# Kernel tuning notes

Hardware: AMD Instinct MI355X
Metric: run time of the kernel (lower is better)

## Reference

```python
import jax, jax.numpy as jnp
import numpy as np
import math

B, S, D, H = 2, 2048, 768, 12
HD = D // H


def setup_inputs() -> dict:
    key = jax.random.key(0)
    ks = jax.random.split(key, 9)
    scale = 1.0 / math.sqrt(D)
    x = jax.random.normal(ks[0], (B, S, D), dtype=jnp.float32)
    # causal mask: True where attention is allowed (query i attends to key j<=i)
    mask = jnp.tril(jnp.ones((S, S), dtype=bool))[None, None]  # [1,1,S,S]
    wq = jax.random.normal(ks[1], (D, D), dtype=jnp.float32) * scale
    bq = jnp.zeros((D,), dtype=jnp.float32)
    wk = jax.random.normal(ks[2], (D, D), dtype=jnp.float32) * scale
    bk = jnp.zeros((D,), dtype=jnp.float32)
    wv = jax.random.normal(ks[3], (D, D), dtype=jnp.float32) * scale
    bv = jnp.zeros((D,), dtype=jnp.float32)
    wo = jax.random.normal(ks[4], (D, D), dtype=jnp.float32) * scale
    bo = jnp.zeros((D,), dtype=jnp.float32)
    return {"x": x, "mask": mask, "wq": wq, "bq": bq, "wk": wk, "bk": bk,
            "wv": wv, "bv": bv, "wo": wo, "bo": bo}


def reference(x, mask, wq, bq, wk, bk, wv, bv, wo, bo):
    b, s, d = x.shape
    # projections (flax Linear: y = x @ kernel + bias)
    q = (x @ wq + bq).reshape(b, s, H, HD).transpose(0, 2, 1, 3)  # [b,h,s,hd]
    k = (x @ wk + bk).reshape(b, s, H, HD).transpose(0, 2, 1, 3)
    v = (x @ wv + bv).reshape(b, s, H, HD).transpose(0, 2, 1, 3)
    scores = jnp.einsum('bhqd,bhkd->bhqk', q, k) / math.sqrt(HD)  # [b,h,s,s]
    scores = jnp.where(mask, scores, -jnp.inf)
    attn = jax.nn.softmax(scores, axis=-1)
    out = jnp.einsum('bhqk,bhkd->bhqd', attn, v)  # [b,h,s,hd]
    out = out.transpose(0, 2, 1, 3).reshape(b, s, d)
    return out @ wo + bo
```

## Files before the change

### kernel.cpp

```cpp
#include <hip/hip_runtime.h>
#include <math.h>

#define BATCH 2
#define SEQ   2048
#define DMODEL 768
#define NHEAD 12
#define HDIM  64

typedef unsigned short u16;
typedef __attribute__((ext_vector_type(8))) short bf16x8;
typedef __attribute__((ext_vector_type(4))) float f32x4;
typedef __attribute__((ext_vector_type(8))) unsigned short us8;
typedef __attribute__((ext_vector_type(4))) unsigned short us4;

__device__ __forceinline__ u16 f2bf(float f) {
    union { float f; unsigned u; } v; v.f = f;
    unsigned u = v.u;
    u += 0x7fff + ((u >> 16) & 1);
    return (u16)(u >> 16);
}

__device__ __forceinline__ void g2l16(const void* g, void* l) {
    __builtin_amdgcn_global_load_lds(
        (const __attribute__((address_space(1))) unsigned int*)g,
        (__attribute__((address_space(3))) unsigned int*)(unsigned int)(unsigned long long)(uintptr_t)l,
        16, 0, 0);
}

__global__ __launch_bounds__(256) void prep(const float* __restrict__ x,
                                            const float* __restrict__ w0,
                                            const float* __restrict__ w1,
                                            const float* __restrict__ w2,
                                            const float* __restrict__ w3,
                                            u16* __restrict__ xb,
                                            u16* __restrict__ Wt_all) {
    __shared__ float t[32][33];
    const int bid = blockIdx.x;
    if (bid < 3072) {
        int i = bid * 256 + threadIdx.x;
        float4 v = ((const float4*)x)[i];
        us4 o;
        o.x = f2bf(v.x); o.y = f2bf(v.y); o.z = f2bf(v.z); o.w = f2bf(v.w);
        *(us4*)&xb[(size_t)i * 4] = o;
    } else {
        const int wid = bid - 3072;
        const int z  = wid / 576;
        const int rr = wid % 576;
        const int by = rr / 24, bx = rr % 24;
        const float* W = z == 0 ? w0 : z == 1 ? w1 : z == 2 ? w2 : w3;
        u16* Wt = Wt_all + (size_t)z * DMODEL * DMODEL;

        int tx = threadIdx.x & 31, ty = threadIdx.x >> 5;
        int xg = bx * 32 + tx;
        #pragma unroll
        for (int j = 0; j < 32; j += 8)
            t[ty + j][tx] = W[(size_t)(by * 32 + ty + j) * DMODEL + xg];
        __syncthreads();
        int x2 = by * 32 + tx;
        #pragma unroll
        for (int j = 0; j < 32; j += 8)
            Wt[(size_t)(bx * 32 + ty + j) * DMODEL + x2] = f2bf(t[tx][ty + j]);
    }
}

__device__ __forceinline__ void mfma_loop(const u16* __restrict__ Ag,
                                          const u16* __restrict__ Bt,
                                          int m0, int n0, int tid,
                                          u16* As, u16* Bs,
                                          f32x4 acc[4][4]) {
    const int lane = tid & 63;
    const int quad = lane >> 4, l16 = lane & 15;
    const int w    = tid >> 6;
    const int wm   = w >> 1, wn = w & 1;
    const int rowA = tid >> 2;
    const int kch  = (tid & 3) * 8;

    for (int k0 = 0; k0 < DMODEL; k0 += 32) {
        const u16* Agk = Ag + (size_t)m0 * DMODEL + k0;
        const u16* Btk = Bt + (size_t)n0 * DMODEL + k0;
        g2l16(Agk + (size_t)rowA * DMODEL + kch,        As + tid * 8);
        g2l16(Agk + (size_t)(rowA + 64) * DMODEL + kch, As + 2048 + tid * 8);
        g2l16(Btk + (size_t)rowA * DMODEL + kch,        Bs + tid * 8);
        g2l16(Btk + (size_t)(rowA + 64) * DMODEL + kch, Bs + 2048 + tid * 8);
        __syncthreads();

        bf16x8 af[4], bfr[4];
        #pragma unroll
        for (int i = 0; i < 4; ++i)
            af[i] = *(const bf16x8*)&As[(wm * 64 + i * 16 + l16) * 32 + quad * 8];
        #pragma unroll
        for (int j = 0; j < 4; ++j)
            bfr[j] = *(const bf16x8*)&Bs[(wn * 64 + j * 16 + l16) * 32 + quad * 8];
        #pragma unroll
        for (int i = 0; i < 4; ++i)
            #pragma unroll
            for (int j = 0; j < 4; ++j)
                acc[i][j] = __builtin_amdgcn_mfma_f32_16x16x32_bf16(af[i], bfr[j], acc[i][j], 0, 0, 0);
        __syncthreads();
    }
}

__global__ __launch_bounds__(256) void gemm_qkv(
    const u16* __restrict__ xb, const u16* __restrict__ WtQK,
    const u16* __restrict__ WtV,
    const float* __restrict__ bq, const float* __restrict__ bk,
    const float* __restrict__ bv,
    u16* __restrict__ QK, u16* __restrict__ Vt) {

    __shared__ __align__(16) u16 As[128 * 32];
    __shared__ __align__(16) u16 Bs[128 * 32];

    const int tid  = threadIdx.x;
    const int lane = tid & 63;
    const int w    = tid >> 6;
    const int quad = lane >> 4, l16 = lane & 15;
    const int wm   = w >> 1, wn = w & 1;
    const int bid  = blockIdx.x;

    f32x4 acc[4][4] = {};

    if (bid < 384) {
        const int m0 = (bid & 31) * 128, n0 = (bid >> 5) * 128;
        mfma_loop(xb, WtQK, m0, n0, tid, As, Bs, acc);

        const size_t n_elem = (size_t)BATCH * SEQ * DMODEL;
        #pragma unroll
        for (int j = 0; j < 4; ++j) {
            const int n     = n0 + wn * 64 + j * 16 + l16;
            const int which = n / 768;
            const int nn    = n - which * 768;
            const float bias  = (which == 0 ? bq : bk)[nn];
            const float scale = (which == 0) ? 0.125f : 1.0f;
            const int h = nn >> 6, hd = nn & 63;
            u16* outw = QK + (size_t)which * n_elem;
            #pragma unroll
            for (int i = 0; i < 4; ++i) {
                const int mbase = m0 + wm * 64 + i * 16 + quad * 4;
                #pragma unroll
                for (int r = 0; r < 4; ++r) {
                    const int m  = mbase + r;
                    const int b_ = m >> 11, s_ = m & 2047;
                    outw[(size_t)((b_ * NHEAD + h) * SEQ + s_) * HDIM + hd] =
                        f2bf((acc[i][j][r] + bias) * scale);
                }
            }
        }
    } else {
        const int vid = bid - 384;
        const int m0 = (vid % 6) * 128, n0 = (vid / 6) * 128;
        mfma_loop(WtV, xb, m0, n0, tid, As, Bs, acc);

        #pragma unroll
        for (int i = 0; i < 4; ++i) {
            const int rbase = m0 + wm * 64 + i * 16 + quad * 4;
            #pragma unroll
            for (int r = 0; r < 4; ++r) {
                const int row_g = rbase + r;
                const float bias = bv[row_g];
                const int h = row_g >> 6, hd = row_g & 63;
                #pragma unroll
                for (int j = 0; j < 4; ++j) {
                    const int col_g = n0 + wn * 64 + j * 16 + l16;
                    const int b_ = col_g >> 11, s_ = col_g & 2047;
                    Vt[(size_t)((b_ * NHEAD + h) * HDIM + hd) * SEQ + s_] =
                        f2bf(acc[i][j][r] + bias);
                }
            }
        }
    }
}

__global__ __launch_bounds__(256) void gemm_out(
    const u16* __restrict__ Ag, const u16* __restrict__ Bt,
    const float* __restrict__ bo, float* __restrict__ out) {

    __shared__ __align__(16) u16 As[128 * 32];
    __shared__ __align__(16) u16 Bs[128 * 32];

    const int tid  = threadIdx.x;
    const int lane = tid & 63;
    const int w    = tid >> 6;
    const int quad = lane >> 4, l16 = lane & 15;
    const int wm   = w >> 1, wn = w & 1;
    const int m0 = blockIdx.x * 128, n0 = blockIdx.y * 128;

    f32x4 acc[4][4] = {};
    mfma_loop(Ag, Bt, m0, n0, tid, As, Bs, acc);

    #pragma unroll
    for (int i = 0; i < 4; ++i) {
        const int mbase = m0 + wm * 64 + i * 16 + quad * 4;
        #pragma unroll
        for (int r = 0; r < 4; ++r) {
            const int m = mbase + r;
            #pragma unroll
            for (int j = 0; j < 4; ++j) {
                const int n = n0 + wn * 64 + j * 16 + l16;
                out[(size_t)m * DMODEL + n] = acc[i][j][r] + bo[n];
            }
        }
    }
}

__global__ __launch_bounds__(256) void flash_attn_mfma(
    const u16* __restrict__ Q, const u16* __restrict__ K,
    const u16* __restrict__ Vt, u16* __restrict__ A) {

    __shared__ __align__(16) u16 Kl[64 * 72];
    __shared__ __align__(16) u16 Vl[64 * 72];
    __shared__ __align__(16) u16 Pl[4][16 * 72];

    const int tid  = threadIdx.x;
    const int lane = tid & 63;
    const int w    = tid >> 6;
    const int quad = lane >> 4;
    const int l16  = lane & 15;

    const int p  = blockIdx.x;
    const int bh = blockIdx.y;
    const int uq = (w < 2) ? p : 63 - p;
    const int wrow0 = uq * 32 + (w & 1) * 16;
    const int wlast = wrow0 + 15;

    const size_t base = (size_t)bh * SEQ * HDIM;
    const u16* Qg = Q + base;
    const u16* Kg = K + base;
    const u16* Vg = Vt + base;

    bf16x8 qf0 = *(const bf16x8*)&Qg[(size_t)(wrow0 + l16) * 64 + quad * 8];
    bf16x8 qf1 = *(const bf16x8*)&Qg[(size_t)(wrow0 + l16) * 64 + quad * 8 + 32];

    f32x4 o[4] = {};
    float l_acc[4] = {0.f, 0.f, 0.f, 0.f};

    const int qrow = wrow0 + quad * 4;
    const int uB = 63 - p;
    const int tcount = (32 * uB + 31) / 64 + 1;

    for (int t2 = 0; t2 < tcount; ++t2) {
        const int j0 = t2 * 64;
        __syncthreads();

        #pragma unroll
        for (int r = 0; r < 2; ++r) {
            int e = tid + r * 256;
            int row = e >> 3, col = (e & 7) * 8;
            *(us8*)&Kl[row * 72 + col] = *(const us8*)&Kg[(size_t)(j0 + row) * 64 + col];
        }
        #pragma unroll
        for (int r = 0; r < 2; ++r) {
            int e = tid + r * 256;
            int d = e >> 3, kc = (e & 7) * 8;
            *(us8*)&Vl[d * 72 + kc] = *(const us8*)&Vg[(size_t)d * SEQ + j0 + kc];
        }
        __syncthreads();

        if (j0 > wlast) continue;

        f32x4 s[4];
        #pragma unroll
        for (int c = 0; c < 4; ++c) {
            bf16x8 kf0 = *(const bf16x8*)&Kl[(c * 16 + l16) * 72 + quad * 8];
            bf16x8 kf1 = *(const bf16x8*)&Kl[(c * 16 + l16) * 72 + quad * 8 + 32];
            f32x4 a2 = {};
            a2 = __builtin_amdgcn_mfma_f32_16x16x32_bf16(qf0, kf0, a2, 0, 0, 0);
            a2 = __builtin_amdgcn_mfma_f32_16x16x32_bf16(qf1, kf1, a2, 0, 0, 0);
            s[c] = a2;
        }

        if (j0 + 63 > wrow0) {
            #pragma unroll
            for (int c = 0; c < 4; ++c) {
                int jg = j0 + c * 16 + l16;
                #pragma unroll
                for (int r = 0; r < 4; ++r)
                    if (jg > qrow + r) s[c][r] = -INFINITY;
            }
        }

        #pragma unroll
        for (int c = 0; c < 4; ++c)
            #pragma unroll
            for (int r = 0; r < 4; ++r)
                s[c][r] = __expf(s[c][r]);
        #pragma unroll
        for (int r = 0; r < 4; ++r)
            l_acc[r] += (s[0][r] + s[1][r]) + (s[2][r] + s[3][r]);

        u16* Pw = Pl[w];
        #pragma unroll
        for (int c = 0; c < 4; ++c)
            #pragma unroll
            for (int r = 0; r < 4; ++r)
                Pw[(quad * 4 + r) * 72 + c * 16 + l16] = f2bf(s[c][r]);
        bf16x8 pf0 = *(const bf16x8*)&Pw[l16 * 72 + quad * 8];
        bf16x8 pf1 = *(const bf16x8*)&Pw[l16 * 72 + quad * 8 + 32];

        #pragma unroll
        for (int c2 = 0; c2 < 4; ++c2) {
            bf16x8 vf0 = *(const bf16x8*)&Vl[(c2 * 16 + l16) * 72 + quad * 8];
            bf16x8 vf1 = *(const bf16x8*)&Vl[(c2 * 16 + l16) * 72 + quad * 8 + 32];
            o[c2] = __builtin_amdgcn_mfma_f32_16x16x32_bf16(pf0, vf0, o[c2], 0, 0, 0);
            o[c2] = __builtin_amdgcn_mfma_f32_16x16x32_bf16(pf1, vf1, o[c2], 0, 0, 0);
        }
    }

    #pragma unroll
    for (int off = 1; off < 16; off <<= 1)
        #pragma unroll
        for (int r = 0; r < 4; ++r)
            l_acc[r] += __shfl_xor(l_acc[r], off);

    const int b = bh / NHEAD, h = bh % NHEAD;
    #pragma unroll
    for (int r = 0; r < 4; ++r) {
        float inv = 1.0f / l_acc[r];
        int sg = qrow + r;
        u16* dst = A + ((size_t)(b * SEQ + sg)) * DMODEL + h * HDIM;
        #pragma unroll
        for (int c2 = 0; c2 < 4; ++c2)
            dst[c2 * 16 + l16] = f2bf(o[c2][r] * inv);
    }
}

extern "C" void kernel_launch(void* const* d_in, const int* in_sizes, int n_in,
                              void* d_out, int out_size, void* d_ws, size_t ws_size,
                              hipStream_t stream) {
    const float* x  = (const float*)d_in[0];
    const float* wq = (const float*)d_in[2];
    const float* bq = (const float*)d_in[3];
    const float* wk = (const float*)d_in[4];
    const float* bk = (const float*)d_in[5];
    const float* wv = (const float*)d_in[6];
    const float* bv = (const float*)d_in[7];
    const float* wo = (const float*)d_in[8];
    const float* bo = (const float*)d_in[9];
    float* out = (float*)d_out;

    const size_t n_elem = (size_t)BATCH * SEQ * DMODEL;
    const size_t w_elem = (size_t)DMODEL * DMODEL;

    u16* xb     = (u16*)d_ws;
    u16* Wt_all = xb + n_elem;
    u16* Qw     = Wt_all + 4 * w_elem;
    u16* Kw     = Qw + n_elem;
    u16* Vtw    = Kw + n_elem;
    u16* Aw     = Vtw + n_elem;

    dim3 blk(256);

    prep<<<dim3(3072 + 2304), blk, 0, stream>>>(x, wq, wk, wv, wo, xb, Wt_all);

    gemm_qkv<<<dim3(384 + 192), blk, 0, stream>>>(xb, Wt_all,
                                                  Wt_all + 2 * w_elem,
                                                  bq, bk, bv, Qw, Vtw);

    flash_attn_mfma<<<dim3(32, 24), blk, 0, stream>>>(Qw, Kw, Vtw, Aw);

    gemm_out<<<dim3(32, 6), blk, 0, stream>>>(Aw, Wt_all + 3 * w_elem, bo, out);
}
```

Before: 193.2 us.

## Restructure flash attention into single-wave blocks and shrink output GEMM tiles

New measurement: 213.6 us. +10.6%, slower.

```diff
diff --git a/kernel.cpp b/kernel.cpp
--- a/kernel.cpp
+++ b/kernel.cpp
@@ -174,152 +174,222 @@
     const u16* __restrict__ Ag, const u16* __restrict__ Bt,
     const float* __restrict__ bo, float* __restrict__ out) {
 
-    __shared__ __align__(16) u16 As[128 * 32];
-    __shared__ __align__(16) u16 Bs[128 * 32];
+    __shared__ __align__(16) u16 As[64 * 32];
+    __shared__ __align__(16) u16 Bs[64 * 32];
 
     const int tid  = threadIdx.x;
     const int lane = tid & 63;
     const int w    = tid >> 6;
     const int quad = lane >> 4, l16 = lane & 15;
     const int wm   = w >> 1, wn = w & 1;
-    const int m0 = blockIdx.x * 128, n0 = blockIdx.y * 128;
-
-    f32x4 acc[4][4] = {};
-    mfma_loop(Ag, Bt, m0, n0, tid, As, Bs, acc);
+    const int m0 = blockIdx.x * 64, n0 = blockIdx.y * 64;
+
+    const int rowA = tid >> 2;
+    const int kch  = (tid & 3) * 8;
+
+    f32x4 acc[2][2] = {};
+
+    for (int k0 = 0; k0 < DMODEL; k0 += 32) {
+        g2l16(Ag + (size_t)(m0 + rowA) * DMODEL + k0 + kch, As + tid * 8);
+        g2l16(Bt + (size_t)(n0 + rowA) * DMODEL + k0 + kch, Bs + tid * 8);
+        __syncthreads();
+
+        bf16x8 af[2], bfr[2];
+        #pragma unroll
+        for (int i = 0; i < 2; ++i)
+            af[i] = *(const bf16x8*)&As[(wm * 32 + i * 16 + l16) * 32 + quad * 8];
+        #pragma unroll
+        for (int j = 0; j < 2; ++j)
+            bfr[j] = *(const bf16x8*)&Bs[(wn * 32 + j * 16 + l16) * 32 + quad * 8];
+        #pragma unroll
+        for (int i = 0; i < 2; ++i)
+            #pragma unroll
+            for (int j = 0; j < 2; ++j)
+                acc[i][j] = __builtin_amdgcn_mfma_f32_16x16x32_bf16(af[i], bfr[j], acc[i][j], 0, 0, 0);
+        __syncthreads();
+    }
 
     #pragma unroll
-    for (int i = 0; i < 4; ++i) {
-        const int mbase = m0 + wm * 64 + i * 16 + quad * 4;
+    for (int i = 0; i < 2; ++i) {
+        const int mbase = m0 + wm * 32 + i * 16 + quad * 4;
         #pragma unroll
         for (int r = 0; r < 4; ++r) {
             const int m = mbase + r;
             #pragma unroll
-            for (int j = 0; j < 4; ++j) {
-                const int n = n0 + wn * 64 + j * 16 + l16;
+            for (int j = 0; j < 2; ++j) {
+                const int n = n0 + wn * 32 + j * 16 + l16;
                 out[(size_t)m * DMODEL + n] = acc[i][j][r] + bo[n];
             }
         }
     }
 }
 
-__global__ __launch_bounds__(256) void flash_attn_mfma(
+__global__ __launch_bounds__(64) void flash_attn_mfma(
     const u16* __restrict__ Q, const u16* __restrict__ K,
     const u16* __restrict__ Vt, u16* __restrict__ A) {
 
-    __shared__ __align__(16) u16 Kl[64 * 72];
-    __shared__ __align__(16) u16 Vl[64 * 72];
-    __shared__ __align__(16) u16 Pl[4][16 * 72];
-
-    const int tid  = threadIdx.x;
-    const int lane = tid & 63;
-    const int w    = tid >> 6;
+    __shared__ __align__(16) u16 Pl[16 * 72];
+
+    const int lane = threadIdx.x;
     const int quad = lane >> 4;
     const int l16  = lane & 15;
 
-    const int p  = blockIdx.x;
-    const int bh = blockIdx.y;
-    const int uq = (w < 2) ? p : 63 - p;
-    const int wrow0 = uq * 32 + (w & 1) * 16;
-    const int wlast = wrow0 + 15;
+    const int bid = blockIdx.x;
+    const int j   = bid >> 8;
+    const int c   = bid & 255;
+    const int v   = c & 63;
+    const int g   = c >> 6;
+    const int bh  = j * 4 + g;
+    const int rot = (j >> 1) * 21;
+    const int vr  = (v + rot) & 63;
+    const int u   = (j & 1) ? (63 - vr) : vr;
+
+    const int rs = u * 16;
+    const int rb = 2032 - rs;
+    const int slast = rs + 15;
 
     const size_t base = (size_t)bh * SEQ * HDIM;
     const u16* Qg = Q + base;
     const u16* Kg = K + base;
     const u16* Vg = Vt + base;
 
-    bf16x8 qf0 = *(const bf16x8*)&Qg[(size_t)(wrow0 + l16) * 64 + quad * 8];
-    bf16x8 qf1 = *(const bf16x8*)&Qg[(size_t)(wrow0 + l16) * 64 + quad * 8 + 32];
-
-    f32x4 o[4] = {};
-    float l_acc[4] = {0.f, 0.f, 0.f, 0.f};
-
-    const int qrow = wrow0 + quad * 4;
-    const int uB = 63 - p;
-    const int tcount = (32 * uB + 31) / 64 + 1;
-
-    for (int t2 = 0; t2 < tcount; ++t2) {
+    bf16x8 qs0 = *(const bf16x8*)&Qg[(size_t)(rs + l16) * 64 + quad * 8];
+    bf16x8 qs1 = *(const bf16x8*)&Qg[(size_t)(rs + l16) * 64 + quad * 8 + 32];
+    bf16x8 qb0 = *(const bf16x8*)&Qg[(size_t)(rb + l16) * 64 + quad * 8];
+    bf16x8 qb1 = *(const bf16x8*)&Qg[(size_t)(rb + l16) * 64 + quad * 8 + 32];
+
+    f32x4 ob[4] = {}, os[4] = {};
+    float lb[4] = {0.f, 0.f, 0.f, 0.f};
+    float ls[4] = {0.f, 0.f, 0.f, 0.f};
+
+    const int tc = ((rb + 15) >> 6) + 1;
+
+    for (int t2 = 0; t2 < tc; ++t2) {
         const int j0 = t2 * 64;
-        __syncthreads();
-
-        #pragma unroll
-        for (int r = 0; r < 2; ++r) {
-            int e = tid + r * 256;
-            int row = e >> 3, col = (e & 7) * 8;
-            *(us8*)&Kl[row * 72 + col] = *(const us8*)&Kg[(size_t)(j0 + row) * 64 + col];
-        }
-        #pragma unroll
-        for (int r = 0; r < 2; ++r) {
-            int e = tid + r * 256;
-            int d = e >> 3, kc = (e & 7) * 8;
-            *(us8*)&Vl[d * 72 + kc] = *(const us8*)&Vg[(size_t)d * SEQ + j0 + kc];
-        }
-        __syncthreads();
-
-        if (j0 > wlast) continue;
-
-        f32x4 s[4];
-        #pragma unroll
-        for (int c = 0; c < 4; ++c) {
-            bf16x8 kf0 = *(const bf16x8*)&Kl[(c * 16 + l16) * 72 + quad * 8];
-            bf16x8 kf1 = *(const bf16x8*)&Kl[(c * 16 + l16) * 72 + quad * 8 + 32];
-            f32x4 a2 = {};
-            a2 = __builtin_amdgcn_mfma_f32_16x16x32_bf16(qf0, kf0, a2, 0, 0, 0);
-            a2 = __builtin_amdgcn_mfma_f32_16x16x32_bf16(qf1, kf1, a2, 0, 0, 0);
-            s[c] = a2;
-        }
-
-        if (j0 + 63 > wrow0) {
-            #pragma unroll
-            for (int c = 0; c < 4; ++c) {
-                int jg = j0 + c * 16 + l16;
+
+        bf16x8 kf[8], vf[8];
+        #pragma unroll
+        for (int c4 = 0; c4 < 4; ++c4) {
+            const u16* kp = &Kg[(size_t)(j0 + c4 * 16 + l16) * 64 + quad * 8];
+            kf[c4 * 2]     = *(const bf16x8*)kp;
+            kf[c4 * 2 + 1] = *(const bf16x8*)(kp + 32);
+            const u16* vp = &Vg[(size_t)(c4 * 16 + l16) * SEQ + j0 + quad * 8];
+            vf[c4 * 2]     = *(const bf16x8*)vp;
+            vf[c4 * 2 + 1] = *(const bf16x8*)(vp + 32);
+        }
+
+        {
+            f32x4 s[4];
+            #pragma unroll
+            for (int c4 = 0; c4 < 4; ++c4) {
+                f32x4 a2 = {};
+                a2 = __builtin_amdgcn_mfma_f32_16x16x32_bf16(qb0, kf[c4 * 2],     a2, 0, 0, 0);
+                a2 = __builtin_amdgcn_mfma_f32_16x16x32_bf16(qb1, kf[c4 * 2 + 1], a2, 0, 0, 0);
+                s[c4] = a2;
+            }
+            if (j0 + 63 > rb) {
+                #pragma unroll
+                for (int c4 = 0; c4 < 4; ++c4) {
+                    int jg = j0 + c4 * 16 + l16;
+                    #pragma unroll
+                    for (int r = 0; r < 4; ++r)
+                        if (jg > rb + quad * 4 + r) s[c4][r] = -INFINITY;
+                }
+            }
+            #pragma unroll
+            for (int c4 = 0; c4 < 4; ++c4)
                 #pragma unroll
                 for (int r = 0; r < 4; ++r)
-                    if (jg > qrow + r) s[c][r] = -INFINITY;
-            }
-        }
-
-        #pragma unroll
-        for (int c = 0; c < 4; ++c)
+                    s[c4][r] = __expf(s[c4][r]);
             #pragma unroll
             for (int r = 0; r < 4; ++r)
-                s[c][r] = __expf(s[c][r]);
-        #pragma unroll
-        for (int r = 0; r < 4; ++r)
-            l_acc[r] += (s[0][r] + s[1][r]) + (s[2][r] + s[3][r]);
-
-        u16* Pw = Pl[w];
-        #pragma unroll
-        for (int c = 0; c < 4; ++c)
+                lb[r] += (s[0][r] + s[1][r]) + (s[2][r] + s[3][r]);
+
+            #pragma unroll
+            for (int c4 = 0; c4 < 4; ++c4)
+                #pragma unroll
+                for (int r = 0; r < 4; ++r)
+                    Pl[(quad * 4 + r) * 72 + c4 * 16 + l16] = f2bf(s[c4][r]);
+            bf16x8 pf0 = *(const bf16x8*)&Pl[l16 * 72 + quad * 8];
+            bf16x8 pf1 = *(const bf16x8*)&Pl[l16 * 72 + quad * 8 + 32];
+
+            #pragma unroll
+            for (int c2 = 0; c2 < 4; ++c2) {
+                ob[c2] = __builtin_amdgcn_mfma_f32_16x16x32_bf16(pf0, vf[c2 * 2],     ob[c2], 0, 0, 0);
+                ob[c2] = __builtin_amdgcn_mfma_f32_16x16x32_bf16(pf1, vf[c2 * 2 + 1], ob[c2], 0, 0, 0);
+            }
+        }
+
+        if (j0 <= slast) {
+            f32x4 s[4];
+            #pragma unroll
+            for (int c4 = 0; c4 < 4; ++c4) {
+                f32x4 a2 = {};
+                a2 = __builtin_amdgcn_mfma_f32_16x16x32_bf16(qs0, kf[c4 * 2],     a2, 0, 0, 0);
+                a2 = __builtin_amdgcn_mfma_f32_16x16x32_bf16(qs1, kf[c4 * 2 + 1], a2, 0, 0, 0);
+                s[c4] = a2;
+            }
+            if (j0 + 63 > rs) {
+                #pragma unroll
+                for (int c4 = 0; c4 < 4; ++c4) {
+                    int jg = j0 + c4 * 16 + l16;
+                    #pragma unroll
+                    for (int r = 0; r < 4; ++r)
+                        if (jg > rs + quad * 4 + r) s[c4][r] = -INFINITY;
+                }
+            }
+            #pragma unroll
+            for (int c4 = 0; c4 < 4; ++c4)
+                #pragma unroll
+                for (int r = 0; r < 4; ++r)
+                    s[c4][r] = __expf(s[c4][r]);
             #pragma unroll
             for (int r = 0; r < 4; ++r)
-                Pw[(quad * 4 + r) * 72 + c * 16 + l16] = f2bf(s[c][r]);
-        bf16x8 pf0 = *(const bf16x8*)&Pw[l16 * 72 + quad * 8];
-        bf16x8 pf1 = *(const bf16x8*)&Pw[l16 * 72 + quad * 8 + 32];
-
-        #pragma unroll
-        for (int c2 = 0; c2 < 4; ++c2) {
-            bf16x8 vf0 = *(const bf16x8*)&Vl[(c2 * 16 + l16) * 72 + quad * 8];
-            bf16x8 vf1 = *(const bf16x8*)&Vl[(c2 * 16 + l16) * 72 + quad * 8 + 32];
-            o[c2] = __builtin_amdgcn_mfma_f32_16x16x32_bf16(pf0, vf0, o[c2], 0, 0, 0);
-            o[c2] = __builtin_amdgcn_mfma_f32_16x16x32_bf16(pf1, vf1, o[c2], 0, 0, 0);
+                ls[r] += (s[0][r] + s[1][r]) + (s[2][r] + s[3][r]);
+
+            #pragma unroll
+            for (int c4 = 0; c4 < 4; ++c4)
+                #pragma unroll
+                for (int r = 0; r < 4; ++r)
+                    Pl[(quad * 4 + r) * 72 + c4 * 16 + l16] = f2bf(s[c4][r]);
+            bf16x8 pf0 = *(const bf16x8*)&Pl[l16 * 72 + quad * 8];
+            bf16x8 pf1 = *(const bf16x8*)&Pl[l16 * 72 + quad * 8 + 32];
+
+            #pragma unroll
+            for (int c2 = 0; c2 < 4; ++c2) {
+                os[c2] = __builtin_amdgcn_mfma_f32_16x16x32_bf16(pf0, vf[c2 * 2],     os[c2], 0, 0, 0);
+                os[c2] = __builtin_amdgcn_mfma_f32_16x16x32_bf16(pf1, vf[c2 * 2 + 1], os[c2], 0, 0, 0);
+            }
         }
     }
 
     #pragma unroll
     for (int off = 1; off < 16; off <<= 1)
         #pragma unroll
-        for (int r = 0; r < 4; ++r)
-            l_acc[r] += __shfl_xor(l_acc[r], off);
+        for (int r = 0; r < 4; ++r) {
+            lb[r] += __shfl_xor(lb[r], off);
+            ls[r] += __shfl_xor(ls[r], off);
+        }
 
     const int b = bh / NHEAD, h = bh % NHEAD;
     #pragma unroll
     for (int r = 0; r < 4; ++r) {
-        float inv = 1.0f / l_acc[r];
-        int sg = qrow + r;
-        u16* dst = A + ((size_t)(b * SEQ + sg)) * DMODEL + h * HDIM;
-        #pragma unroll
-        for (int c2 = 0; c2 < 4; ++c2)
-            dst[c2 * 16 + l16] = f2bf(o[c2][r] * inv);
+        {
+            float inv = 1.0f / lb[r];
+            int sg = rb + quad * 4 + r;
+            u16* dst = A + ((size_t)(b * SEQ + sg)) * DMODEL + h * HDIM;
+            #pragma unroll
+            for (int c2 = 0; c2 < 4; ++c2)
+                dst[c2 * 16 + l16] = f2bf(ob[c2][r] * inv);
+        }
+        {
+            float inv = 1.0f / ls[r];
+            int sg = rs + quad * 4 + r;
+            u16* dst = A + ((size_t)(b * SEQ + sg)) * DMODEL + h * HDIM;
+            #pragma unroll
+            for (int c2 = 0; c2 < 4; ++c2)
+                dst[c2 * 16 + l16] = f2bf(os[c2][r] * inv);
+        }
     }
 }
 
@@ -355,7 +425,7 @@
                                                   Wt_all + 2 * w_elem,
                                                   bq, bk, bv, Qw, Vtw);
 
-    flash_attn_mfma<<<dim3(32, 24), blk, 0, stream>>>(Qw, Kw, Vtw, Aw);
-
-    gemm_out<<<dim3(32, 6), blk, 0, stream>>>(Aw, Wt_all + 3 * w_elem, bo, out);
-}
+    flash_attn_mfma<<<dim3(1536), dim3(64), 0, stream>>>(Qw, Kw, Vtw, Aw);
+
+    gemm_out<<<dim3(64, 12), blk, 0, stream>>>(Aw, Wt_all + 3 * w_elem, bo, out);
+}
```

## Shrink attention blocks to two waves with rotated causal pairing; smaller output GEMM tiles

Applied to the files above, without the earlier changes.

Measured after the change: 194.4 us. No clear change (+0.7%).

```diff
diff --git a/kernel.cpp b/kernel.cpp
--- a/kernel.cpp
+++ b/kernel.cpp
@@ -174,41 +174,63 @@
     const u16* __restrict__ Ag, const u16* __restrict__ Bt,
     const float* __restrict__ bo, float* __restrict__ out) {
 
-    __shared__ __align__(16) u16 As[128 * 32];
-    __shared__ __align__(16) u16 Bs[128 * 32];
+    __shared__ __align__(16) u16 As[64 * 32];
+    __shared__ __align__(16) u16 Bs[64 * 32];
 
     const int tid  = threadIdx.x;
     const int lane = tid & 63;
     const int w    = tid >> 6;
     const int quad = lane >> 4, l16 = lane & 15;
     const int wm   = w >> 1, wn = w & 1;
-    const int m0 = blockIdx.x * 128, n0 = blockIdx.y * 128;
-
-    f32x4 acc[4][4] = {};
-    mfma_loop(Ag, Bt, m0, n0, tid, As, Bs, acc);
+    const int m0 = blockIdx.x * 64, n0 = blockIdx.y * 64;
+
+    const int rowA = tid >> 2;
+    const int kch  = (tid & 3) * 8;
+
+    f32x4 acc[2][2] = {};
+
+    for (int k0 = 0; k0 < DMODEL; k0 += 32) {
+        g2l16(Ag + (size_t)(m0 + rowA) * DMODEL + k0 + kch, As + tid * 8);
+        g2l16(Bt + (size_t)(n0 + rowA) * DMODEL + k0 + kch, Bs + tid * 8);
+        __syncthreads();
+
+        bf16x8 af[2], bfr[2];
+        #pragma unroll
+        for (int i = 0; i < 2; ++i)
+            af[i] = *(const bf16x8*)&As[(wm * 32 + i * 16 + l16) * 32 + quad * 8];
+        #pragma unroll
+        for (int j = 0; j < 2; ++j)
+            bfr[j] = *(const bf16x8*)&Bs[(wn * 32 + j * 16 + l16) * 32 + quad * 8];
+        #pragma unroll
+        for (int i = 0; i < 2; ++i)
+            #pragma unroll
+            for (int j = 0; j < 2; ++j)
+                acc[i][j] = __builtin_amdgcn_mfma_f32_16x16x32_bf16(af[i], bfr[j], acc[i][j], 0, 0, 0);
+        __syncthreads();
+    }
 
     #pragma unroll
-    for (int i = 0; i < 4; ++i) {
-        const int mbase = m0 + wm * 64 + i * 16 + quad * 4;
+    for (int i = 0; i < 2; ++i) {
+        const int mbase = m0 + wm * 32 + i * 16 + quad * 4;
         #pragma unroll
         for (int r = 0; r < 4; ++r) {
             const int m = mbase + r;
             #pragma unroll
-            for (int j = 0; j < 4; ++j) {
-                const int n = n0 + wn * 64 + j * 16 + l16;
+            for (int j = 0; j < 2; ++j) {
+                const int n = n0 + wn * 32 + j * 16 + l16;
                 out[(size_t)m * DMODEL + n] = acc[i][j][r] + bo[n];
             }
         }
     }
 }
 
-__global__ __launch_bounds__(256) void flash_attn_mfma(
+__global__ __launch_bounds__(128) void flash_attn_mfma(
     const u16* __restrict__ Q, const u16* __restrict__ K,
     const u16* __restrict__ Vt, u16* __restrict__ A) {
 
     __shared__ __align__(16) u16 Kl[64 * 72];
     __shared__ __align__(16) u16 Vl[64 * 72];
-    __shared__ __align__(16) u16 Pl[4][16 * 72];
+    __shared__ __align__(16) u16 Pl[2][16 * 72];
 
     const int tid  = threadIdx.x;
     const int lane = tid & 63;
@@ -216,10 +238,16 @@
     const int quad = lane >> 4;
     const int l16  = lane & 15;
 
-    const int p  = blockIdx.x;
-    const int bh = blockIdx.y;
-    const int uq = (w < 2) ? p : 63 - p;
-    const int wrow0 = uq * 32 + (w & 1) * 16;
+    const int bid = blockIdx.x;
+    const int ch  = bid >> 8;
+    const int c   = bid & 255;
+    const int v   = c & 63;
+    const int bh  = ch * 4 + (c >> 6);
+    const int rot = (ch >> 1) * 21;
+    const int vr  = (v + rot) & 63;
+    const int u   = (ch & 1) ? (63 - vr) : vr;
+
+    const int wrow0 = w ? (127 - u) * 16 : u * 16;
     const int wlast = wrow0 + 15;
 
     const size_t base = (size_t)bh * SEQ * HDIM;
@@ -234,22 +262,21 @@
     float l_acc[4] = {0.f, 0.f, 0.f, 0.f};
 
     const int qrow = wrow0 + quad * 4;
-    const int uB = 63 - p;
-    const int tcount = (32 * uB + 31) / 64 + 1;
-
-    for (int t2 = 0; t2 < tcount; ++t2) {
+    const int tc = (((127 - u) * 16 + 15) >> 6) + 1;
+
+    for (int t2 = 0; t2 < tc; ++t2) {
         const int j0 = t2 * 64;
         __syncthreads();
 
         #pragma unroll
-        for (int r = 0; r < 2; ++r) {
-            int e = tid + r * 256;
+        for (int r = 0; r < 4; ++r) {
+            int e = tid + r * 128;
             int row = e >> 3, col = (e & 7) * 8;
             *(us8*)&Kl[row * 72 + col] = *(const us8*)&Kg[(size_t)(j0 + row) * 64 + col];
         }
         #pragma unroll
-        for (int r = 0; r < 2; ++r) {
-            int e = tid + r * 256;
+        for (int r = 0; r < 4; ++r) {
+            int e = tid + r * 128;
             int d = e >> 3, kc = (e & 7) * 8;
             *(us8*)&Vl[d * 72 + kc] = *(const us8*)&Vg[(size_t)d * SEQ + j0 + kc];
         }
@@ -259,40 +286,40 @@
 
         f32x4 s[4];
         #pragma unroll
-        for (int c = 0; c < 4; ++c) {
-            bf16x8 kf0 = *(const bf16x8*)&Kl[(c * 16 + l16) * 72 + quad * 8];
-            bf16x8 kf1 = *(const bf16x8*)&Kl[(c * 16 + l16) * 72 + quad * 8 + 32];
+        for (int c4 = 0; c4 < 4; ++c4) {
+            bf16x8 kf0 = *(const bf16x8*)&Kl[(c4 * 16 + l16) * 72 + quad * 8];
+            bf16x8 kf1 = *(const bf16x8*)&Kl[(c4 * 16 + l16) * 72 + quad * 8 + 32];
             f32x4 a2 = {};
             a2 = __builtin_amdgcn_mfma_f32_16x16x32_bf16(qf0, kf0, a2, 0, 0, 0);
             a2 = __builtin_amdgcn_mfma_f32_16x16x32_bf16(qf1, kf1, a2, 0, 0, 0);
-            s[c] = a2;
+            s[c4] = a2;
         }
 
         if (j0 + 63 > wrow0) {
             #pragma unroll
-            for (int c = 0; c < 4; ++c) {
-                int jg = j0 + c * 16 + l16;
+            for (int c4 = 0; c4 < 4; ++c4) {
+                int jg = j0 + c4 * 16 + l16;
                 #pragma unroll
                 for (int r = 0; r < 4; ++r)
-                    if (jg > qrow + r) s[c][r] = -INFINITY;
+                    if (jg > qrow + r) s[c4][r] = -INFINITY;
             }
         }
 
         #pragma unroll
-        for (int c = 0; c < 4; ++c)
+        for (int c4 = 0; c4 < 4; ++c4)
             #pragma unroll
             for (int r = 0; r < 4; ++r)
-                s[c][r] = __expf(s[c][r]);
+                s[c4][r] = __expf(s[c4][r]);
         #pragma unroll
         for (int r = 0; r < 4; ++r)
             l_acc[r] += (s[0][r] + s[1][r]) + (s[2][r] + s[3][r]);
 
         u16* Pw = Pl[w];
         #pragma unroll
-        for (int c = 0; c < 4; ++c)
+        for (int c4 = 0; c4 < 4; ++c4)
             #pragma unroll
             for (int r = 0; r < 4; ++r)
-                Pw[(quad * 4 + r) * 72 + c * 16 + l16] = f2bf(s[c][r]);
+                Pw[(quad * 4 + r) * 72 + c4 * 16 + l16] = f2bf(s[c4][r]);
         bf16x8 pf0 = *(const bf16x8*)&Pw[l16 * 72 + quad * 8];
         bf16x8 pf1 = *(const bf16x8*)&Pw[l16 * 72 + quad * 8 + 32];
 
@@ -355,7 +382,7 @@
                                                   Wt_all + 2 * w_elem,
                                                   bq, bk, bv, Qw, Vtw);
 
-    flash_attn_mfma<<<dim3(32, 24), blk, 0, stream>>>(Qw, Kw, Vtw, Aw);
-
-    gemm_out<<<dim3(32, 6), blk, 0, stream>>>(Aw, Wt_all + 3 * w_elem, bo, out);
-}
+    flash_attn_mfma<<<dim3(1536), dim3(128), 0, stream>>>(Qw, Kw, Vtw, Aw);
+
+    gemm_out<<<dim3(64, 12), blk, 0, stream>>>(Aw, Wt_all + 3 * w_elem, bo, out);
+}
```
